# Kernel tuning notes

Hardware: AMD Instinct MI355X
Metric: run time of the kernel (lower is better)

The kernel has to match this reference:

```python
import jax, jax.numpy as jnp
import numpy as np

E, T, H, I, K = 32, 2048, 1024, 512, 4


def setup_inputs() -> dict:
    key = jax.random.key(0)
    k1, k2, k3, k4, k5 = jax.random.split(key, 5)
    hidden_states = jax.random.normal(k1, (T, H), dtype=jnp.float32)
    top_k_index = jax.random.randint(k2, (T, K), 0, E)
    w = jax.random.uniform(k3, (T, K), dtype=jnp.float32)
    top_k_weights = w / jnp.sum(w, axis=-1, keepdims=True)  # router-like normalized weights
    gate_up_proj = jax.random.normal(k4, (E, 2 * I, H), dtype=jnp.float32) * 0.02
    down_proj = jax.random.normal(k5, (E, H, I), dtype=jnp.float32) * 0.02
    return {
        "hidden_states": hidden_states,
        "top_k_index": top_k_index,
        "top_k_weights": top_k_weights,
        "gate_up_proj": gate_up_proj,
        "down_proj": down_proj,
    }


def reference(hidden_states, top_k_index, top_k_weights, gate_up_proj, down_proj):
    # Faithful to the eager MoE dispatch loop: for each expert e, gather the
    # tokens routed to it, run gate/up/down SwiGLU, scale by routing weight,
    # and scatter-add into the output. Expressed as a scan over experts with a
    # per-token routing weight that is 0 for unrouted tokens (identical math:
    # index_add over (token, slot) pairs == sum_k where(idx==e, w, 0)).
    num_experts = gate_up_proj.shape[0]
    inter = down_proj.shape[2]

    def expert_step(acc, xs):
        gup_w, down_w, e = xs  # [2I, H], [H, I], scalar expert id
        # combined routing weight per token for this expert: [T]
        w_tok = jnp.sum(jnp.where(top_k_index == e, top_k_weights, 0.0), axis=1)
        gu = hidden_states @ gup_w.T              # [T, 2I]
        gate, up = gu[:, :inter], gu[:, inter:]
        h = jax.nn.silu(gate) * up                # [T, I]
        out = h @ down_w.T                        # [T, H]
        return acc + out * w_tok[:, None], None

    init = jnp.zeros_like(hidden_states)
    final_hidden_states, _ = jax.lax.scan(
        expert_step, init,
        (gate_up_proj, down_proj, jnp.arange(num_experts)),
    )
    return final_hidden_states
```

## Files before the change

kernel.cpp:

```cpp
#include <hip/hip_runtime.h>

#define NE 32
#define NT 2048
#define NH 1024
#define NI 512
#define NK 4
#define CAP 512

typedef __attribute__((ext_vector_type(8))) short short8;
typedef __attribute__((ext_vector_type(4))) float floatx4;

static __device__ __forceinline__ unsigned pk_bf16(float x, float y) {
#if __has_builtin(__builtin_amdgcn_cvt_pk_bf16_f32)
    typedef __attribute__((ext_vector_type(2))) __bf16 bf16x2;
    union { bf16x2 v; unsigned u; } c;
    c.v = __builtin_amdgcn_cvt_pk_bf16_f32(x, y);
    return c.u;
#else
    union { float f; unsigned u; } a, b;
    a.f = x; b.f = y;
    unsigned ua = (a.u + 0x7fffu + ((a.u >> 16) & 1u)) >> 16;
    unsigned ub = (b.u + 0x7fffu + ((b.u >> 16) & 1u)) >> 16;
    return (ua & 0xffffu) | (ub << 16);
#endif
}

static __device__ __forceinline__ unsigned short bf16_1(float x) {
    return (unsigned short)(pk_bf16(x, 0.f) & 0xffffu);
}

__global__ void route_kernel(const int* __restrict__ idx,
                             const float* __restrict__ w,
                             int* __restrict__ counts,
                             int* __restrict__ tok,
                             float* __restrict__ wgt) {
    int tid = blockIdx.x * blockDim.x + threadIdx.x;
    if (tid >= NT * NK) return;
    int e = idx[tid];
    int pos = atomicAdd(&counts[e], 1);
    if (pos < CAP) {
        tok[e * CAP + pos] = tid;
        wgt[e * CAP + pos] = w[tid];
    }
}

__global__ void cvt_bf16(const float* __restrict__ src,
                         unsigned short* __restrict__ dst, int n8) {
    int i = blockIdx.x * 256 + threadIdx.x;
    if (i >= n8) return;
    size_t o = (size_t)i * 8;
    float4 a = *(const float4*)(src + o);
    float4 b = *(const float4*)(src + o + 4);
    union { unsigned u[4]; short8 s; } c;
    c.u[0] = pk_bf16(a.x, a.y);
    c.u[1] = pk_bf16(a.z, a.w);
    c.u[2] = pk_bf16(b.x, b.y);
    c.u[3] = pk_bf16(b.z, b.w);
    *(short8*)(dst + o) = c.s;
}


__global__ __launch_bounds__(256, 3) void gateup_mfma(
    const unsigned short* __restrict__ hb16,
    const unsigned short* __restrict__ gupb,
    const int* __restrict__ counts,
    const int* __restrict__ tok,
    unsigned short* __restrict__ hbuf)
{
    int e = blockIdx.z;
    int cnt = counts[e]; if (cnt > CAP) cnt = CAP;
    int m0 = blockIdx.y * 128;
    if (m0 >= cnt) return;
    int j0 = blockIdx.x * 64;

    __shared__ __align__(16) short As[128][64];
    __shared__ __align__(16) short Bs[128][64];

    int tid = threadIdx.x;
    int sr = tid >> 3;
    int sg = tid & 7;

    const unsigned short* aptr[4];
    const unsigned short* bptr[4];
    short* awr[4];
    short* bwr[4];
    const unsigned short* gup_e = gupb + (size_t)e * (2 * NI) * NH;
#pragma unroll
    for (int p = 0; p < 4; p++) {
        int r = p * 32 + sr;
        int mi = m0 + r;
        int tk = tok[e * CAP + (mi < cnt ? mi : m0)];
        aptr[p] = hb16 + (size_t)(tk >> 2) * NH + sg * 8;
        awr[p]  = &As[r][(sg ^ (r & 7)) * 8];
        int gj = (r < 64) ? (j0 + r) : (NI + j0 + (r - 64));
        bptr[p] = gup_e + (size_t)gj * NH + sg * 8;
        bwr[p]  = &Bs[r][(sg ^ (r & 7)) * 8];
    }

    int wave = tid >> 6, lane = tid & 63;
    int wm = wave >> 1;
    int wj = wave & 1;
    int lcol = lane & 15;
    int quad = lane >> 4;

    floatx4 acc[4][4];
#pragma unroll
    for (int a = 0; a < 4; a++)
#pragma unroll
        for (int b = 0; b < 4; b++) acc[a][b] = (floatx4){0.f, 0.f, 0.f, 0.f};

    short8 ra[4], rbs[4];
#pragma unroll
    for (int p = 0; p < 4; p++) {
        ra[p]  = *(const short8*)(aptr[p]);
        rbs[p] = *(const short8*)(bptr[p]);
    }

    const int NIT = NH / 64;
    for (int it = 0; it < NIT; ++it) {
        if (it > 0) __syncthreads();
#pragma unroll
        for (int p = 0; p < 4; p++) {
            *(short8*)(awr[p]) = ra[p];
            *(short8*)(bwr[p]) = rbs[p];
        }
        __syncthreads();
        if (it + 1 < NIT) {
            int h = (it + 1) * 64;
#pragma unroll
            for (int p = 0; p < 4; p++) {
                ra[p]  = *(const short8*)(aptr[p] + h);
                rbs[p] = *(const short8*)(bptr[p] + h);
            }
        }
#pragma unroll
        for (int ks = 0; ks < 2; ks++) {
            short8 af[4], bfr[4];
            int q = ks * 4 + quad;
#pragma unroll
            for (int mt = 0; mt < 4; mt++) {
                int R = wm * 64 + mt * 16 + lcol;
                af[mt] = *(const short8*)&As[R][(q ^ (R & 7)) * 8];
            }
#pragma unroll
            for (int nt = 0; nt < 4; nt++) {
                int R = (nt < 2) ? (wj * 32 + nt * 16 + lcol)
                                 : (64 + wj * 32 + (nt - 2) * 16 + lcol);
                bfr[nt] = *(const short8*)&Bs[R][(q ^ (R & 7)) * 8];
            }
#pragma unroll
            for (int mt = 0; mt < 4; mt++)
#pragma unroll
                for (int nt = 0; nt < 4; nt++)
                    acc[mt][nt] = __builtin_amdgcn_mfma_f32_16x16x32_bf16(
                        af[mt], bfr[nt], acc[mt][nt], 0, 0, 0);
        }
    }

#pragma unroll
    for (int mt = 0; mt < 4; mt++) {
#pragma unroll
        for (int i = 0; i < 4; i++) {
            int m = wm * 64 + mt * 16 + quad * 4 + i;
            if (m0 + m < cnt) {
                int tk = tok[e * CAP + m0 + m];
                unsigned short* hp = hbuf + (size_t)tk * NI + j0 + wj * 32 + lcol;
#pragma unroll
                for (int nt = 0; nt < 2; nt++) {
                    float g = acc[mt][nt][i];
                    float u = acc[mt][nt + 2][i];
                    float h = g / (1.f + __expf(-g)) * u;
                    hp[nt * 16] = bf16_1(h);
                }
            }
        }
    }
}

__global__ __launch_bounds__(256, 3) void down_mfma(
    const unsigned short* __restrict__ hbuf,
    const unsigned short* __restrict__ dwnb,
    const int* __restrict__ counts,
    const int* __restrict__ tok,
    const float* __restrict__ wgt,
    float* __restrict__ out)
{
    int e = blockIdx.z;
    int cnt = counts[e]; if (cnt > CAP) cnt = CAP;
    int m0 = blockIdx.y * 128;
    if (m0 >= cnt) return;
    int n0 = blockIdx.x * 128;

    __shared__ __align__(16) short As[128][64];
    __shared__ __align__(16) short Bs[128][64];

    int tid = threadIdx.x;
    int sr = tid >> 3;
    int sg = tid & 7;

    const unsigned short* aptr[4];
    const unsigned short* bptr[4];
    short* awr[4];
    short* bwr[4];
    const unsigned short* dwn_e = dwnb + (size_t)e * NH * NI;
#pragma unroll
    for (int p = 0; p < 4; p++) {
        int r = p * 32 + sr;
        int mi = m0 + r;
        int tk = tok[e * CAP + (mi < cnt ? mi : m0)];
        aptr[p] = hbuf + (size_t)tk * NI + sg * 8;
        awr[p]  = &As[r][(sg ^ (r & 7)) * 8];
        bptr[p] = dwn_e + (size_t)(n0 + r) * NI + sg * 8;
        bwr[p]  = &Bs[r][(sg ^ (r & 7)) * 8];
    }

    int wave = tid >> 6, lane = tid & 63;
    int wm = wave >> 1, wn = wave & 1;
    int lcol = lane & 15;
    int quad = lane >> 4;

    floatx4 acc[4][4];
#pragma unroll
    for (int a = 0; a < 4; a++)
#pragma unroll
        for (int b = 0; b < 4; b++) acc[a][b] = (floatx4){0.f, 0.f, 0.f, 0.f};

    short8 ra[4], rbs[4];
#pragma unroll
    for (int p = 0; p < 4; p++) {
        ra[p]  = *(const short8*)(aptr[p]);
        rbs[p] = *(const short8*)(bptr[p]);
    }

    const int NIT = NI / 64;
    for (int it = 0; it < NIT; ++it) {
        if (it > 0) __syncthreads();
#pragma unroll
        for (int p = 0; p < 4; p++) {
            *(short8*)(awr[p]) = ra[p];
            *(short8*)(bwr[p]) = rbs[p];
        }
        __syncthreads();
        if (it + 1 < NIT) {
            int h = (it + 1) * 64;
#pragma unroll
            for (int p = 0; p < 4; p++) {
                ra[p]  = *(const short8*)(aptr[p] + h);
                rbs[p] = *(const short8*)(bptr[p] + h);
            }
        }
#pragma unroll
        for (int ks = 0; ks < 2; ks++) {
            short8 af[4], bfr[4];
            int q = ks * 4 + quad;
#pragma unroll
            for (int mt = 0; mt < 4; mt++) {
                int R = wm * 64 + mt * 16 + lcol;
                af[mt] = *(const short8*)&As[R][(q ^ (R & 7)) * 8];
            }
#pragma unroll
            for (int nt = 0; nt < 4; nt++) {
                int R = wn * 64 + nt * 16 + lcol;
                bfr[nt] = *(const short8*)&Bs[R][(q ^ (R & 7)) * 8];
            }
#pragma unroll
            for (int mt = 0; mt < 4; mt++)
#pragma unroll
                for (int nt = 0; nt < 4; nt++)
                    acc[mt][nt] = __builtin_amdgcn_mfma_f32_16x16x32_bf16(
                        af[mt], bfr[nt], acc[mt][nt], 0, 0, 0);
        }
    }

#pragma unroll
    for (int mt = 0; mt < 4; mt++)
#pragma unroll
        for (int i = 0; i < 4; i++) {
            int m = wm * 64 + mt * 16 + quad * 4 + i;
            if (m0 + m < cnt) {
                int tk = tok[e * CAP + m0 + m];
                float wl = wgt[e * CAP + m0 + m];
                float* op = out + (size_t)(tk >> 2) * NH + n0 + wn * 64 + lcol;
#pragma unroll
                for (int nt = 0; nt < 4; nt++)
                    atomicAdd(op + nt * 16, acc[mt][nt][i] * wl);
            }
        }
}

extern "C" void kernel_launch(void* const* d_in, const int* in_sizes, int n_in,
                              void* d_out, int out_size, void* d_ws, size_t ws_size,
                              hipStream_t stream) {
    const float* hidden = (const float*)d_in[0];
    const int*   tk_idx = (const int*)d_in[1];
    const float* tk_w   = (const float*)d_in[2];
    const float* gup    = (const float*)d_in[3];
    const float* down   = (const float*)d_in[4];
    float* out = (float*)d_out;

    char* ws = (char*)d_ws;
    size_t off = 0;
    int*            counts = (int*)(ws + off); off += 256;
    int*            tok    = (int*)(ws + off); off += (size_t)NE * CAP * 4;
    float*          wgt    = (float*)(ws + off); off += (size_t)NE * CAP * 4;
    unsigned short* hb16   = (unsigned short*)(ws + off); off += (size_t)NT * NH * 2;
    unsigned short* hbuf   = (unsigned short*)(ws + off); off += (size_t)NT * NK * NI * 2;
    unsigned short* gupb   = (unsigned short*)(ws + off); off += (size_t)NE * 2 * NI * NH * 2;
    unsigned short* dwnb   = (unsigned short*)(ws + off); off += (size_t)NE * NH * NI * 2;

    hipMemsetAsync(counts, 0, 256, stream);
    hipMemsetAsync(out, 0, (size_t)NT * NH * sizeof(float), stream);

    route_kernel<<<(NT * NK + 255) / 256, 256, 0, stream>>>(tk_idx, tk_w, counts, tok, wgt);

    int n8_h = NT * NH / 8;
    cvt_bf16<<<(n8_h + 255) / 256, 256, 0, stream>>>(hidden, hb16, n8_h);
    int n8_g = NE * 2 * NI * NH / 8;
    cvt_bf16<<<(n8_g + 255) / 256, 256, 0, stream>>>(gup, gupb, n8_g);
    int n8_d = NE * NH * NI / 8;
    cvt_bf16<<<(n8_d + 255) / 256, 256, 0, stream>>>(down, dwnb, n8_d);

    dim3 gridG(NI / 64, CAP / 128, NE);
    gateup_mfma<<<gridG, 256, 0, stream>>>(hb16, gupb, counts, tok, hbuf);

    dim3 gridD(NH / 128, CAP / 128, NE);
    down_mfma<<<gridD, 256, 0, stream>>>(hbuf, dwnb, counts, tok, wgt, out);
}
```

Baseline: 370.1 us.

## Fuse fp32-to-bf16 weight conversion into GEMM loads and drop LDS staging

```diff
diff --git a/kernel.cpp b/kernel.cpp
--- a/kernel.cpp
+++ b/kernel.cpp
@@ -29,6 +29,15 @@
     return (unsigned short)(pk_bf16(x, 0.f) & 0xffffu);
 }
 
+static __device__ __forceinline__ short8 cvt_frag(float4 lo, float4 hi) {
+    union { unsigned u[4]; short8 s; } c;
+    c.u[0] = pk_bf16(lo.x, lo.y);
+    c.u[1] = pk_bf16(lo.z, lo.w);
+    c.u[2] = pk_bf16(hi.x, hi.y);
+    c.u[3] = pk_bf16(hi.z, hi.w);
+    return c.s;
+}
+
 __global__ void route_kernel(const int* __restrict__ idx,
                              const float* __restrict__ w,
                              int* __restrict__ counts,
@@ -44,25 +53,18 @@
     }
 }
 
-__global__ void cvt_bf16(const float* __restrict__ src,
-                         unsigned short* __restrict__ dst, int n8) {
-    int i = blockIdx.x * 256 + threadIdx.x;
-    if (i >= n8) return;
-    size_t o = (size_t)i * 8;
-    float4 a = *(const float4*)(src + o);
-    float4 b = *(const float4*)(src + o + 4);
-    union { unsigned u[4]; short8 s; } c;
-    c.u[0] = pk_bf16(a.x, a.y);
-    c.u[1] = pk_bf16(a.z, a.w);
-    c.u[2] = pk_bf16(b.x, b.y);
-    c.u[3] = pk_bf16(b.z, b.w);
-    *(short8*)(dst + o) = c.s;
+__global__ void cvt_hidden(const float* __restrict__ hidden,
+                           unsigned short* __restrict__ hb16) {
+    size_t o = (size_t)(blockIdx.x * 256 + threadIdx.x) * 8;
+    float4 a = *(const float4*)(hidden + o);
+    float4 b = *(const float4*)(hidden + o + 4);
+    *(short8*)(hb16 + o) = cvt_frag(a, b);
 }
 
 
 __global__ __launch_bounds__(256, 3) void gateup_mfma(
     const unsigned short* __restrict__ hb16,
-    const unsigned short* __restrict__ gupb,
+    const float* __restrict__ gup,
     const int* __restrict__ counts,
     const int* __restrict__ tok,
     unsigned short* __restrict__ hbuf)
@@ -73,88 +75,53 @@
     if (m0 >= cnt) return;
     int j0 = blockIdx.x * 64;
 
-    __shared__ __align__(16) short As[128][64];
-    __shared__ __align__(16) short Bs[128][64];
-
     int tid = threadIdx.x;
-    int sr = tid >> 3;
-    int sg = tid & 7;
-
-    const unsigned short* aptr[4];
-    const unsigned short* bptr[4];
-    short* awr[4];
-    short* bwr[4];
-    const unsigned short* gup_e = gupb + (size_t)e * (2 * NI) * NH;
-#pragma unroll
-    for (int p = 0; p < 4; p++) {
-        int r = p * 32 + sr;
-        int mi = m0 + r;
-        int tk = tok[e * CAP + (mi < cnt ? mi : m0)];
-        aptr[p] = hb16 + (size_t)(tk >> 2) * NH + sg * 8;
-        awr[p]  = &As[r][(sg ^ (r & 7)) * 8];
-        int gj = (r < 64) ? (j0 + r) : (NI + j0 + (r - 64));
-        bptr[p] = gup_e + (size_t)gj * NH + sg * 8;
-        bwr[p]  = &Bs[r][(sg ^ (r & 7)) * 8];
-    }
-
     int wave = tid >> 6, lane = tid & 63;
     int wm = wave >> 1;
     int wj = wave & 1;
     int lcol = lane & 15;
     int quad = lane >> 4;
 
+    const unsigned short* aptr[4];
+#pragma unroll
+    for (int mt = 0; mt < 4; mt++) {
+        int m = m0 + wm * 64 + mt * 16 + lcol;
+        int row = tok[e * CAP + (m < cnt ? m : m0)];
+        aptr[mt] = hb16 + (size_t)(row >> 2) * NH + quad * 8;
+    }
+    const float* bptr[4];
+    const float* gup_e = gup + (size_t)e * (2 * NI) * NH;
+#pragma unroll
+    for (int nt = 0; nt < 2; nt++) {
+        int j = j0 + wj * 32 + nt * 16 + lcol;
+        bptr[nt]     = gup_e + (size_t)j * NH + quad * 8;
+        bptr[nt + 2] = gup_e + (size_t)(NI + j) * NH + quad * 8;
+    }
+
     floatx4 acc[4][4];
 #pragma unroll
     for (int a = 0; a < 4; a++)
 #pragma unroll
         for (int b = 0; b < 4; b++) acc[a][b] = (floatx4){0.f, 0.f, 0.f, 0.f};
 
-    short8 ra[4], rbs[4];
-#pragma unroll
-    for (int p = 0; p < 4; p++) {
-        ra[p]  = *(const short8*)(aptr[p]);
-        rbs[p] = *(const short8*)(bptr[p]);
-    }
-
-    const int NIT = NH / 64;
-    for (int it = 0; it < NIT; ++it) {
-        if (it > 0) __syncthreads();
-#pragma unroll
-        for (int p = 0; p < 4; p++) {
-            *(short8*)(awr[p]) = ra[p];
-            *(short8*)(bwr[p]) = rbs[p];
-        }
-        __syncthreads();
-        if (it + 1 < NIT) {
-            int h = (it + 1) * 64;
-#pragma unroll
-            for (int p = 0; p < 4; p++) {
-                ra[p]  = *(const short8*)(aptr[p] + h);
-                rbs[p] = *(const short8*)(bptr[p] + h);
-            }
-        }
-#pragma unroll
-        for (int ks = 0; ks < 2; ks++) {
-            short8 af[4], bfr[4];
-            int q = ks * 4 + quad;
-#pragma unroll
-            for (int mt = 0; mt < 4; mt++) {
-                int R = wm * 64 + mt * 16 + lcol;
-                af[mt] = *(const short8*)&As[R][(q ^ (R & 7)) * 8];
-            }
-#pragma unroll
-            for (int nt = 0; nt < 4; nt++) {
-                int R = (nt < 2) ? (wj * 32 + nt * 16 + lcol)
-                                 : (64 + wj * 32 + (nt - 2) * 16 + lcol);
-                bfr[nt] = *(const short8*)&Bs[R][(q ^ (R & 7)) * 8];
-            }
-#pragma unroll
-            for (int mt = 0; mt < 4; mt++)
-#pragma unroll
-                for (int nt = 0; nt < 4; nt++)
-                    acc[mt][nt] = __builtin_amdgcn_mfma_f32_16x16x32_bf16(
-                        af[mt], bfr[nt], acc[mt][nt], 0, 0, 0);
-        }
+#pragma unroll 2
+    for (int k = 0; k < NH; k += 32) {
+        short8 af[4], bfr[4];
+#pragma unroll
+        for (int mt = 0; mt < 4; mt++)
+            af[mt] = *(const short8*)(aptr[mt] + k);
+#pragma unroll
+        for (int nt = 0; nt < 4; nt++) {
+            float4 lo = *(const float4*)(bptr[nt] + k);
+            float4 hi = *(const float4*)(bptr[nt] + k + 4);
+            bfr[nt] = cvt_frag(lo, hi);
+        }
+#pragma unroll
+        for (int mt = 0; mt < 4; mt++)
+#pragma unroll
+            for (int nt = 0; nt < 4; nt++)
+                acc[mt][nt] = __builtin_amdgcn_mfma_f32_16x16x32_bf16(
+                    af[mt], bfr[nt], acc[mt][nt], 0, 0, 0);
     }
 
 #pragma unroll
@@ -179,7 +146,7 @@
 
 __global__ __launch_bounds__(256, 3) void down_mfma(
     const unsigned short* __restrict__ hbuf,
-    const unsigned short* __restrict__ dwnb,
+    const float* __restrict__ down,
     const int* __restrict__ counts,
     const int* __restrict__ tok,
     const float* __restrict__ wgt,
@@ -191,85 +158,51 @@
     if (m0 >= cnt) return;
     int n0 = blockIdx.x * 128;
 
-    __shared__ __align__(16) short As[128][64];
-    __shared__ __align__(16) short Bs[128][64];
-
     int tid = threadIdx.x;
-    int sr = tid >> 3;
-    int sg = tid & 7;
-
-    const unsigned short* aptr[4];
-    const unsigned short* bptr[4];
-    short* awr[4];
-    short* bwr[4];
-    const unsigned short* dwn_e = dwnb + (size_t)e * NH * NI;
-#pragma unroll
-    for (int p = 0; p < 4; p++) {
-        int r = p * 32 + sr;
-        int mi = m0 + r;
-        int tk = tok[e * CAP + (mi < cnt ? mi : m0)];
-        aptr[p] = hbuf + (size_t)tk * NI + sg * 8;
-        awr[p]  = &As[r][(sg ^ (r & 7)) * 8];
-        bptr[p] = dwn_e + (size_t)(n0 + r) * NI + sg * 8;
-        bwr[p]  = &Bs[r][(sg ^ (r & 7)) * 8];
-    }
-
     int wave = tid >> 6, lane = tid & 63;
     int wm = wave >> 1, wn = wave & 1;
     int lcol = lane & 15;
     int quad = lane >> 4;
 
+    const unsigned short* aptr[4];
+#pragma unroll
+    for (int mt = 0; mt < 4; mt++) {
+        int m = m0 + wm * 64 + mt * 16 + lcol;
+        int row = tok[e * CAP + (m < cnt ? m : m0)];
+        aptr[mt] = hbuf + (size_t)row * NI + quad * 8;
+    }
+    const float* bptr[4];
+    const float* dwn_e = down + (size_t)e * NH * NI;
+#pragma unroll
+    for (int nt = 0; nt < 4; nt++) {
+        int n = n0 + wn * 64 + nt * 16 + lcol;
+        bptr[nt] = dwn_e + (size_t)n * NI + quad * 8;
+    }
+
     floatx4 acc[4][4];
 #pragma unroll
     for (int a = 0; a < 4; a++)
 #pragma unroll
         for (int b = 0; b < 4; b++) acc[a][b] = (floatx4){0.f, 0.f, 0.f, 0.f};
 
-    short8 ra[4], rbs[4];
-#pragma unroll
-    for (int p = 0; p < 4; p++) {
-        ra[p]  = *(const short8*)(aptr[p]);
-        rbs[p] = *(const short8*)(bptr[p]);
-    }
-
-    const int NIT = NI / 64;
-    for (int it = 0; it < NIT; ++it) {
-        if (it > 0) __syncthreads();
-#pragma unroll
-        for (int p = 0; p < 4; p++) {
-            *(short8*)(awr[p]) = ra[p];
-            *(short8*)(bwr[p]) = rbs[p];
-        }
-        __syncthreads();
-        if (it + 1 < NIT) {
-            int h = (it + 1) * 64;
-#pragma unroll
-            for (int p = 0; p < 4; p++) {
-                ra[p]  = *(const short8*)(aptr[p] + h);
-                rbs[p] = *(const short8*)(bptr[p] + h);
-            }
-        }
-#pragma unroll
-        for (int ks = 0; ks < 2; ks++) {
-            short8 af[4], bfr[4];
-            int q = ks * 4 + quad;
-#pragma unroll
-            for (int mt = 0; mt < 4; mt++) {
-                int R = wm * 64 + mt * 16 + lcol;
-                af[mt] = *(const short8*)&As[R][(q ^ (R & 7)) * 8];
-            }
-#pragma unroll
-            for (int nt = 0; nt < 4; nt++) {
-                int R = wn * 64 + nt * 16 + lcol;
-                bfr[nt] = *(const short8*)&Bs[R][(q ^ (R & 7)) * 8];
-            }
-#pragma unroll
-            for (int mt = 0; mt < 4; mt++)
-#pragma unroll
-                for (int nt = 0; nt < 4; nt++)
-                    acc[mt][nt] = __builtin_amdgcn_mfma_f32_16x16x32_bf16(
-                        af[mt], bfr[nt], acc[mt][nt], 0, 0, 0);
-        }
+#pragma unroll 2
+    for (int k = 0; k < NI; k += 32) {
+        short8 af[4], bfr[4];
+#pragma unroll
+        for (int mt = 0; mt < 4; mt++)
+            af[mt] = *(const short8*)(aptr[mt] + k);
+#pragma unroll
+        for (int nt = 0; nt < 4; nt++) {
+            float4 lo = *(const float4*)(bptr[nt] + k);
+            float4 hi = *(const float4*)(bptr[nt] + k + 4);
+            bfr[nt] = cvt_frag(lo, hi);
+        }
+#pragma unroll
+        for (int mt = 0; mt < 4; mt++)
+#pragma unroll
+            for (int nt = 0; nt < 4; nt++)
+                acc[mt][nt] = __builtin_amdgcn_mfma_f32_16x16x32_bf16(
+                    af[mt], bfr[nt], acc[mt][nt], 0, 0, 0);
     }
 
 #pragma unroll
@@ -305,24 +238,16 @@
     float*          wgt    = (float*)(ws + off); off += (size_t)NE * CAP * 4;
     unsigned short* hb16   = (unsigned short*)(ws + off); off += (size_t)NT * NH * 2;
     unsigned short* hbuf   = (unsigned short*)(ws + off); off += (size_t)NT * NK * NI * 2;
-    unsigned short* gupb   = (unsigned short*)(ws + off); off += (size_t)NE * 2 * NI * NH * 2;
-    unsigned short* dwnb   = (unsigned short*)(ws + off); off += (size_t)NE * NH * NI * 2;
 
     hipMemsetAsync(counts, 0, 256, stream);
     hipMemsetAsync(out, 0, (size_t)NT * NH * sizeof(float), stream);
 
     route_kernel<<<(NT * NK + 255) / 256, 256, 0, stream>>>(tk_idx, tk_w, counts, tok, wgt);
-
-    int n8_h = NT * NH / 8;
-    cvt_bf16<<<(n8_h + 255) / 256, 256, 0, stream>>>(hidden, hb16, n8_h);
-    int n8_g = NE * 2 * NI * NH / 8;
-    cvt_bf16<<<(n8_g + 255) / 256, 256, 0, stream>>>(gup, gupb, n8_g);
-    int n8_d = NE * NH * NI / 8;
-    cvt_bf16<<<(n8_d + 255) / 256, 256, 0, stream>>>(down, dwnb, n8_d);
+    cvt_hidden<<<(NT * NH / 8) / 256, 256, 0, stream>>>(hidden, hb16);
 
     dim3 gridG(NI / 64, CAP / 128, NE);
-    gateup_mfma<<<gridG, 256, 0, stream>>>(hb16, gupb, counts, tok, hbuf);
+    gateup_mfma<<<gridG, 256, 0, stream>>>(hb16, gup, counts, tok, hbuf);
 
     dim3 gridD(NH / 128, CAP / 128, NE);
-    down_mfma<<<gridD, 256, 0, stream>>>(hbuf, dwnb, counts, tok, wgt, out);
-}
+    down_mfma<<<gridD, 256, 0, stream>>>(hbuf, down, counts, tok, wgt, out);
+}
```

New measurement: 643.1 us. 1.74x slower.
